# Kernel optimization log

Hardware: AMD Instinct MI355X
Metric: run time of the kernel (lower is better)

## Reference

```python
import jax, jax.numpy as jnp
import numpy as np

TEMPERATURE = 10000.0
LN_EPS = 1e-5

def build_freqs(H, W, head_dim):
    # (H*W, head_dim) rotary angles: [theta_h, theta_h, theta_w, theta_w]
    gh, gw = jnp.meshgrid(jnp.arange(H, dtype=jnp.float32), jnp.arange(W, dtype=jnp.float32), indexing='ij')
    dq = head_dim // 4
    freq = 1.0 / (TEMPERATURE ** (jnp.arange(dq, dtype=jnp.float32) / dq))
    th = gh.reshape(-1, 1) * freq[None, :]
    tw = gw.reshape(-1, 1) * freq[None, :]
    return jnp.concatenate([th, th, tw, tw], axis=-1)

def apply_rope(x, freqs):
    # x: (B, nh, N, hd), freqs: (N, hd)
    cos = jnp.cos(freqs)[None, None]
    sin = jnp.sin(freqs)[None, None]
    hd = x.shape[-1]
    x1, x2 = x[..., :hd // 2], x[..., hd // 2:]
    x_rot = jnp.concatenate([-x2, x1], axis=-1)
    return x * cos + x_rot * sin

def setup_inputs() -> dict:
    key = jax.random.key(0)
    ks = jax.random.split(key, 8)
    dim, hidden, B, H, W = 192, 384, 4, 128, 128
    N = H * W
    s = 0.02
    return {
        'x': jax.random.normal(ks[0], (B, N, dim), jnp.float32),
        'in_w': jax.random.normal(ks[1], (hidden, dim), jnp.float32) * s,
        'in_b': jnp.zeros((hidden,), jnp.float32),
        'qkv_w': jax.random.normal(ks[2], (3 * hidden, hidden), jnp.float32) * s,
        'qkv_b': jnp.zeros((3 * hidden,), jnp.float32),
        'lepe_w': jax.random.normal(ks[3], (hidden, 1, 3, 3), jnp.float32) * s,
        'lepe_b': jnp.zeros((hidden,), jnp.float32),
        'ln_g': jnp.ones((hidden,), jnp.float32),
        'ln_b': jnp.zeros((hidden,), jnp.float32),
        'out_w': jax.random.normal(ks[4], (dim, hidden), jnp.float32) * s,
        'out_b': jnp.zeros((dim,), jnp.float32),
        'H': H,
        'W': W,
    }

def reference(x, in_w, in_b, qkv_w, qkv_b, lepe_w, lepe_b, ln_g, ln_b, out_w, out_b, H, W):
    B, N, C = x.shape
    hidden = in_w.shape[0]
    nh = 8
    hd = hidden // nh
    # in_proj: 1x1 conv == per-token linear
    x_seq = jnp.einsum('bnc,hc->bnh', x, in_w) + in_b
    # fused qkv
    qkv = jnp.einsum('bnh,oh->bno', x_seq, qkv_w) + qkv_b
    q, k, v = jnp.split(qkv, 3, axis=-1)
    # LEPE: 3x3 depthwise conv on V in NCHW layout
    v2d = v.transpose(0, 2, 1).reshape(B, hidden, H, W)
    lepe = jax.lax.conv_general_dilated(
        v2d, lepe_w, window_strides=(1, 1), padding=((1, 1), (1, 1)),
        feature_group_count=hidden, dimension_numbers=('NCHW', 'OIHW', 'NCHW'))
    lepe = lepe + lepe_b[None, :, None, None]
    v = v + lepe.reshape(B, hidden, N).transpose(0, 2, 1)
    # split heads -> (B, nh, N, hd)
    q = q.reshape(B, N, nh, hd).transpose(0, 2, 1, 3)
    k = k.reshape(B, N, nh, hd).transpose(0, 2, 1, 3)
    v = v.reshape(B, N, nh, hd).transpose(0, 2, 1, 3)
    freqs = build_freqs(H, W, hd)
    q = apply_rope(q, freqs)
    k = apply_rope(k, freqs)
    # phi = ELU + 1 feature map
    q = jax.nn.elu(q) + 1.0
    k = jax.nn.elu(k) + 1.0
    # linear attention associativity trick
    kv = jnp.einsum('bhnd,bhne->bhde', k, v)
    out = jnp.einsum('bhnd,bhde->bhne', q, kv)
    k_sum = k.sum(axis=2)  # (B, nh, hd)
    denom = jnp.maximum(jnp.einsum('bhnd,bhd->bhn', q, k_sum)[..., None], 1e-6)
    out = out / denom
    out = out.transpose(0, 2, 1, 3).reshape(B, N, hidden)
    # LayerNorm + out_proj
    mu = out.mean(axis=-1, keepdims=True)
    var = out.var(axis=-1, keepdims=True)
    out = (out - mu) * jax.lax.rsqrt(var + LN_EPS) * ln_g + ln_b
    return jnp.einsum('bnh,ch->bnc', out, out_w) + out_b
```

## Files before the change

kernel.cpp:

```cpp
#include <hip/hip_runtime.h>
#include <cstdint>
#include <cstddef>

#define NN_TOK 16384
#define ROWS   65536
#define CDIM   192
#define HID    384
#define NHEAD  8
#define HD     48
#define QKVO   1152

typedef unsigned short ushort_t;
typedef __bf16 bf16x8 __attribute__((ext_vector_type(8)));
typedef float  f32x4  __attribute__((ext_vector_type(4)));

__device__ __forceinline__ ushort_t f2bf(float f) {
  unsigned int u = __float_as_uint(f);
  u += 0x7fffu + ((u >> 16) & 1u);
  return (ushort_t)(u >> 16);
}
__device__ __forceinline__ float bf2f(ushort_t u) {
  return __uint_as_float(((unsigned int)u) << 16);
}

__global__ void cast_x(const float* __restrict__ x, ushort_t* __restrict__ xb, int n8) {
  int i = blockIdx.x * blockDim.x + threadIdx.x;
  if (i >= n8) return;
  const float4* src = (const float4*)(x + (size_t)i * 8);
  float4 f0 = src[0], f1 = src[1];
  uint4 pk;
  pk.x = (unsigned)f2bf(f0.x) | ((unsigned)f2bf(f0.y) << 16);
  pk.y = (unsigned)f2bf(f0.z) | ((unsigned)f2bf(f0.w) << 16);
  pk.z = (unsigned)f2bf(f1.x) | ((unsigned)f2bf(f1.y) << 16);
  pk.w = (unsigned)f2bf(f1.z) | ((unsigned)f2bf(f1.w) << 16);
  *(uint4*)(xb + (size_t)i * 8) = pk;
}

__global__ void combine_w(const float* __restrict__ in_w, const float* __restrict__ in_b,
                          const float* __restrict__ qkv_w, const float* __restrict__ qkv_b,
                          ushort_t* __restrict__ Wcb, float* __restrict__ bc) {
  int o = blockIdx.x;
  int c = threadIdx.x;
  const float* qw = qkv_w + o * HID;
  float s = 0.f;
  for (int m = 0; m < HID; ++m) s += qw[m] * in_w[m * CDIM + c];
  Wcb[o * CDIM + c] = f2bf(s);
  if (c == 0) {
    float sb = qkv_b[o];
    for (int m = 0; m < HID; ++m) sb += qw[m] * in_b[m];
    bc[o] = sb;
  }
}

__global__ void cast_ow(const float* __restrict__ w, ushort_t* __restrict__ wb, int n) {
  int i = blockIdx.x * blockDim.x + threadIdx.x;
  if (i < n) wb[i] = f2bf(w[i]);
}

__global__ void build_tab(float4* __restrict__ tab4) {
  int i = blockIdx.x * blockDim.x + threadIdx.x;
  if (i >= NN_TOK * 24) return;
  int n = i / 24, dp = i - n * 24;
  int j = dp % 12;
  const float c0 = 1.1073093649624542f;
  float freq = exp2f(-(float)j * c0);
  float fy = (float)(n >> 7), fx = (float)(n & 127);
  float s1, c1, s2, c2;
  sincosf(fy * freq, &s1, &c1);
  sincosf(fx * freq, &s2, &c2);
  tab4[i] = make_float4(c1, s1, c2, s2);
}

template<int BM, int BN, int WM, int WN, bool OUTBF16>
__global__ __launch_bounds__(256) void gemm_mfma(const ushort_t* __restrict__ A, int lda,
                                                 const ushort_t* __restrict__ Wb,
                                                 const float* __restrict__ bias,
                                                 void* __restrict__ Cptr,
                                                 int K, int O) {
  constexpr int TM = BM / WM / 16;
  constexpr int TN = BN / WN / 16;
  __shared__ __align__(16) ushort_t As[BM][40];
  __shared__ __align__(16) ushort_t Bs[BN][40];
  const int t    = threadIdx.x;
  const int lane = t & 63;
  const int wave = t >> 6;
  const int quad = lane >> 4;
  const int l15  = lane & 15;
  const int wm   = wave / WN, wn = wave % WN;
  const int m_base = wm * (BM / WM);
  const int n_base = wn * (BN / WN);
  const int n0 = blockIdx.y * BM;
  const int o0 = blockIdx.x * BN;
  f32x4 acc[TM][TN] = {};

  for (int kt = 0; kt < K; kt += 32) {
    for (int c = t; c < BM * 4; c += 256) {
      int row = c >> 2, col8 = (c & 3) * 8;
      *(uint4*)&As[row][col8] = *(const uint4*)(A + (size_t)(n0 + row) * lda + kt + col8);
    }
    for (int c = t; c < BN * 4; c += 256) {
      int row = c >> 2, col8 = (c & 3) * 8;
      *(uint4*)&Bs[row][col8] = *(const uint4*)(Wb + (size_t)(o0 + row) * K + kt + col8);
    }
    __syncthreads();
    bf16x8 af[TM], bfr[TN];
#pragma unroll
    for (int mi = 0; mi < TM; ++mi)
      af[mi] = *(const bf16x8*)&As[m_base + mi * 16 + l15][quad * 8];
#pragma unroll
    for (int ni = 0; ni < TN; ++ni)
      bfr[ni] = *(const bf16x8*)&Bs[n_base + ni * 16 + l15][quad * 8];
#pragma unroll
    for (int mi = 0; mi < TM; ++mi)
#pragma unroll
      for (int ni = 0; ni < TN; ++ni)
        acc[mi][ni] = __builtin_amdgcn_mfma_f32_16x16x32_bf16(af[mi], bfr[ni], acc[mi][ni], 0, 0, 0);
    __syncthreads();
  }
#pragma unroll
  for (int mi = 0; mi < TM; ++mi) {
#pragma unroll
    for (int ni = 0; ni < TN; ++ni) {
      int col = o0 + n_base + ni * 16 + l15;
      float bv = bias[col];
      int rbase = n0 + m_base + mi * 16 + quad * 4;
#pragma unroll
      for (int r = 0; r < 4; ++r) {
        float val = acc[mi][ni][r] + bv;
        if (OUTBF16) ((ushort_t*)Cptr)[(size_t)(rbase + r) * O + col] = f2bf(val);
        else         ((float*)Cptr)[(size_t)(rbase + r) * O + col] = val;
      }
    }
  }
}

__global__ __launch_bounds__(256) void kv_partial_k(const ushort_t* __restrict__ kq,
                                                    const ushort_t* __restrict__ vq,
                                                    const float4* __restrict__ tab4,
                                                    const float* __restrict__ lw,
                                                    const float* __restrict__ lb,
                                                    float* __restrict__ part) {
  const int bid   = blockIdx.x;
  const int chunk = bid & 63;
  const int bh    = bid >> 6;
  const int b     = bh >> 3;
  const int h     = bh & 7;
  const int t     = threadIdx.x;
  const int lane  = t & 63;
  const int wave  = t >> 6;
  __shared__ __align__(16) ushort_t ksF[3][16][16][8];
  __shared__ __align__(16) ushort_t vsF[3][16][16][8];
  __shared__ float wlds[9][48];
  __shared__ float blds[48];
  float* red   = (float*)&ksF[0][0][0][0];
  float* ksred = (float*)&vsF[0][0][0][0];
  for (int c = t; c < 432; c += 256) {
    int ch = c / 9, tap = c - ch * 9;
    wlds[tap][ch] = lw[(h * HD + ch) * 9 + tap];
  }
  if (t < 48) blds[t] = lb[h * HD + t];
  __syncthreads();

  const int g  = lane >> 4;
  const int d0 = lane & 15;
  f32x4 acc[3][3] = {};
  float ksacc = 0.f;
  const int n0 = b * NN_TOK + chunk * 256;

  for (int it = 0; it < 2; ++it) {
    const int nbase = it * 128;
    for (int c = t; c < 384; c += 256) {
      int rr = c / 3, s8 = (c - (c / 3) * 3) * 8;
      int n  = n0 + nbase + rr;
      int nn = n & (NN_TOK - 1);
      const ushort_t* kr = kq + (size_t)n * QKVO + h * HD;
      uint4 ka = *(const uint4*)(kr + s8);
      uint4 kb = *(const uint4*)(kr + s8 + 24);
      ushort_t ua[8], ub[8];
      *(uint4*)ua = ka; *(uint4*)ub = kb;
      const float4* t4 = tab4 + nn * 24 + s8;
      const int nb = rr >> 3, nm = rr & 7;
#pragma unroll
      for (int jj = 0; jj < 8; ++jj) {
        float4 cs = t4[jj];
        float in1 = bf2f(ua[jj]), in2 = bf2f(ub[jj]);
        float o1 = in1 * cs.x - in2 * cs.y;
        float o2 = in2 * cs.z + in1 * cs.w;
        o1 = (o1 > 0.f) ? o1 + 1.f : expf(o1);
        o2 = (o2 > 0.f) ? o2 + 1.f : expf(o2);
        const int d1 = s8 + jj, d2 = s8 + 24 + jj;
        ksF[d1 >> 4][nb][d1 & 15][nm] = f2bf(o1);
        ksF[d2 >> 4][nb][d2 & 15][nm] = f2bf(o2);
      }
    }
    {
      const int nst = chunk * 256 + nbase;
      const int y   = nst >> 7;
      for (int c = t; c < 768; c += 256) {
        int rr = c / 6, gg = c - (c / 6) * 6;
        int x = rr;
        float a8[8], ctr[8];
#pragma unroll
        for (int ci = 0; ci < 8; ++ci) a8[ci] = blds[gg * 8 + ci];
#pragma unroll
        for (int dy = -1; dy <= 1; ++dy) {
#pragma unroll
          for (int dx = -1; dx <= 1; ++dx) {
            int yy = y + dy, xx = x + dx;
            float m = ((unsigned)yy < 128u && (unsigned)xx < 128u) ? 1.f : 0.f;
            int yc = min(max(yy, 0), 127), xc = min(max(xx, 0), 127);
            const ushort_t* src = vq + ((size_t)(b * NN_TOK + (yc << 7) + xc)) * QKVO + h * HD + gg * 8;
            uint4 pk = *(const uint4*)src;
            ushort_t uu[8];
            *(uint4*)uu = pk;
            const int tap = (dy + 1) * 3 + (dx + 1);
#pragma unroll
            for (int ci = 0; ci < 8; ++ci) {
              float val = bf2f(uu[ci]);
              if (dy == 0 && dx == 0) ctr[ci] = val;
              a8[ci] += (wlds[tap][gg * 8 + ci] * m) * val;
            }
          }
        }
        const int nb = rr >> 3, nm = rr & 7;
#pragma unroll
        for (int ci = 0; ci < 8; ++ci) {
          const int e = gg * 8 + ci;
          vsF[e >> 4][nb][e & 15][nm] = f2bf(ctr[ci] + a8[ci]);
        }
      }
    }
    __syncthreads();
    {
      const int w4 = wave * 4 + g;
      bf16x8 af[3], bfr[3];
#pragma unroll
      for (int dg = 0; dg < 3; ++dg) af[dg]  = *(const bf16x8*)&ksF[dg][w4][d0][0];
#pragma unroll
      for (int eg = 0; eg < 3; ++eg) bfr[eg] = *(const bf16x8*)&vsF[eg][w4][d0][0];
#pragma unroll
      for (int dg = 0; dg < 3; ++dg)
#pragma unroll
        for (int eg = 0; eg < 3; ++eg)
          acc[dg][eg] = __builtin_amdgcn_mfma_f32_16x16x32_bf16(af[dg], bfr[eg], acc[dg][eg], 0, 0, 0);
    }
    if (lane < 48) {
      const int dg = lane >> 4, dd = lane & 15;
#pragma unroll 8
      for (int rr = 0; rr < 32; ++rr) {
        int nl = wave * 32 + rr;
        ksacc += bf2f(ksF[dg][nl >> 3][dd][nl & 7]);
      }
    }
    __syncthreads();
  }
  if (wave == 0) {
#pragma unroll
    for (int dg = 0; dg < 3; ++dg)
#pragma unroll
      for (int eg = 0; eg < 3; ++eg)
#pragma unroll
        for (int r = 0; r < 4; ++r)
          red[(dg * 16 + g * 4 + r) * 48 + eg * 16 + d0] = acc[dg][eg][r];
  }
  if (lane < 48) ksred[wave * 48 + lane] = ksacc;
  __syncthreads();
  for (int w = 1; w < 4; ++w) {
    if (wave == w) {
#pragma unroll
      for (int dg = 0; dg < 3; ++dg)
#pragma unroll
        for (int eg = 0; eg < 3; ++eg)
#pragma unroll
          for (int r = 0; r < 4; ++r)
            red[(dg * 16 + g * 4 + r) * 48 + eg * 16 + d0] += acc[dg][eg][r];
    }
    __syncthreads();
  }
  float* p = part + (size_t)bid * 2352;
  for (int c = t; c < 2304; c += 256) p[c] = red[c];
  if (t < 48) p[2304 + t] = ksred[t] + ksred[48 + t] + ksred[96 + t] + ksred[144 + t];
}

__global__ void kv_phase2(const float* __restrict__ part, ushort_t* __restrict__ kvT) {
  int bh  = blockIdx.x >> 3;
  int seg = blockIdx.x & 7;
  int t   = threadIdx.x;
  ushort_t* dst = kvT + (size_t)bh * 8192;
  for (int i = seg * 1024 + t; i < (seg + 1) * 1024; i += 256) {
    int rem = i & 4095, e = rem >> 6, d = rem & 63;
    if (d >= 48 || e >= 49) dst[i] = 0;
  }
  int cend = (seg + 1) * 294;
  for (int c = seg * 294 + t; c < cend; c += 256) {
    const float* p = part + (size_t)(bh * 64) * 2352 + c;
    float s = 0.f;
    for (int ch = 0; ch < 64; ++ch) s += p[(size_t)ch * 2352];
    int d, e;
    if (c < 2304) { d = c / 48; e = c - d * 48; }
    else          { e = 48; d = c - 2304; }
    ushort_t hi = f2bf(s);
    float lo = s - bf2f(hi);
    dst[(size_t)e * 64 + d]        = hi;
    dst[4096 + (size_t)e * 64 + d] = f2bf(lo);
  }
}

__global__ __launch_bounds__(256) void attn_ln_fused(const ushort_t* __restrict__ q,
                                                     const float4* __restrict__ tab4,
                                                     const ushort_t* __restrict__ kvT,
                                                     const float* __restrict__ ln_g,
                                                     const float* __restrict__ ln_b,
                                                     ushort_t* __restrict__ oln) {
  __shared__ __align__(16) ushort_t qsL[32][392];
  __shared__ float lnp[4][32][2];
  const int t    = threadIdx.x;
  const int lane = t & 63;
  const int wave = t >> 6;
  const int quad = lane >> 4;
  const int l15  = lane & 15;
  const int row0 = blockIdx.x * 32;
  const int b    = row0 >> 14;
  const int h0   = wave * 2;
  const float2* tab2 = (const float2*)tab4;

  for (int c = t; c < 1536; c += 256) {
    int r = c / 48, seg = c - (c / 48) * 48;
    *(uint4*)&qsL[r][seg * 8] = *(const uint4*)(q + (size_t)(row0 + r) * QKVO + seg * 8);
  }
  __syncthreads();

  f32x4 acc[2][2][4] = {};

  float gg[2][3], bb[2][3];
#pragma unroll
  for (int hi = 0; hi < 2; ++hi)
#pragma unroll
    for (int nt = 0; nt < 3; ++nt) {
      int col = (h0 + hi) * 48 + nt * 16 + l15;
      gg[hi][nt] = ln_g[col];
      bb[hi][nt] = ln_b[col];
    }

#pragma unroll
  for (int s = 0; s < 2; ++s) {
    const int d0 = s * 32 + quad * 8;
    const bool valid = d0 < 48;
    const bool caseA = d0 < 24;
    const int dp0 = caseA ? d0 : d0 - 24;
    bf16x8 af[2][2] = {};
    if (valid) {
      const int dpart = caseA ? d0 + 24 : d0 - 24;
      const int csel  = caseA ? 0 : 1;
      const float sgn = caseA ? -1.f : 1.f;
#pragma unroll
      for (int m = 0; m < 2; ++m) {
        const int r  = row0 + m * 16 + l15;
        const int nn = r & (NN_TOK - 1);
        float2 cs[8];
#pragma unroll
        for (int j = 0; j < 8; ++j) cs[j] = tab2[(size_t)(nn * 24 + dp0 + j) * 2 + csel];
#pragma unroll
        for (int hi = 0; hi < 2; ++hi) {
          const ushort_t* qr = &qsL[m * 16 + l15][(h0 + hi) * 48];
          uint4 pr = *(const uint4*)(qr + d0);
          uint4 pa = *(const uint4*)(qr + dpart);
          ushort_t up[8], ua[8];
          *(uint4*)up = pr; *(uint4*)ua = pa;
          unsigned w[4];
#pragma unroll
          for (int j2 = 0; j2 < 4; ++j2) {
            float o2[2];
#pragma unroll
            for (int k = 0; k < 2; ++k) {
              int j = j2 * 2 + k;
              float vp = bf2f(up[j]), va = bf2f(ua[j]);
              float o = vp * cs[j].x + va * (sgn * cs[j].y);
              o2[k] = (o > 0.f) ? o + 1.f : expf(o);
            }
            w[j2] = (unsigned)f2bf(o2[0]) | ((unsigned)f2bf(o2[1]) << 16);
          }
          uint4 pk = make_uint4(w[0], w[1], w[2], w[3]);
          af[hi][m] = *(bf16x8*)&pk;
        }
      }
    }
#pragma unroll
    for (int hi = 0; hi < 2; ++hi) {
      const ushort_t* kb = kvT + (size_t)(b * 8 + h0 + hi) * 8192;
#pragma unroll
      for (int nt = 0; nt < 4; ++nt) {
        bf16x8 bH = *(const bf16x8*)(kb + (nt * 16 + l15) * 64 + d0);
        bf16x8 bL = *(const bf16x8*)(kb + 4096 + (nt * 16 + l15) * 64 + d0);
#pragma unroll
        for (int m = 0; m < 2; ++m) {
          acc[hi][m][nt] = __builtin_amdgcn_mfma_f32_16x16x32_bf16(af[hi][m], bH, acc[hi][m][nt], 0, 0, 0);
          acc[hi][m][nt] = __builtin_amdgcn_mfma_f32_16x16x32_bf16(af[hi][m], bL, acc[hi][m][nt], 0, 0, 0);
        }
      }
    }
  }

  float rdn[2][2][4];
#pragma unroll
  for (int hi = 0; hi < 2; ++hi)
#pragma unroll
    for (int m = 0; m < 2; ++m)
#pragma unroll
      for (int r = 0; r < 4; ++r) {
        float dn = __shfl(acc[hi][m][3][r], lane & 48);
        rdn[hi][m][r] = 1.f / fmaxf(dn, 1e-6f);
      }
  float s1[2][4] = {}, s2[2][4] = {};
#pragma unroll
  for (int hi = 0; hi < 2; ++hi)
#pragma unroll
    for (int m = 0; m < 2; ++m)
#pragma unroll
      for (int nt = 0; nt < 3; ++nt)
#pragma unroll
        for (int r = 0; r < 4; ++r) {
          float o = acc[hi][m][nt][r] * rdn[hi][m][r];
          acc[hi][m][nt][r] = o;
          s1[m][r] += o;
          s2[m][r] += o * o;
        }
#pragma unroll
  for (int m = 0; m < 2; ++m)
#pragma unroll
    for (int r = 0; r < 4; ++r) {
#pragma unroll
      for (int msk = 1; msk < 16; msk <<= 1) {
        s1[m][r] += __shfl_xor(s1[m][r], msk, 64);
        s2[m][r] += __shfl_xor(s2[m][r], msk, 64);
      }
    }
  if (l15 == 0) {
#pragma unroll
    for (int m = 0; m < 2; ++m)
#pragma unroll
      for (int r = 0; r < 4; ++r) {
        int rr = m * 16 + quad * 4 + r;
        lnp[wave][rr][0] = s1[m][r];
        lnp[wave][rr][1] = s2[m][r];
      }
  }
  __syncthreads();
  float muv[2][4], rsv[2][4];
#pragma unroll
  for (int m = 0; m < 2; ++m)
#pragma unroll
    for (int r = 0; r < 4; ++r) {
      int rr = m * 16 + quad * 4 + r;
      float a  = lnp[0][rr][0] + lnp[1][rr][0] + lnp[2][rr][0] + lnp[3][rr][0];
      float bq = lnp[0][rr][1] + lnp[1][rr][1] + lnp[2][rr][1] + lnp[3][rr][1];
      float mu  = a * (1.f / 384.f);
      float var = bq * (1.f / 384.f) - mu * mu;
      muv[m][r] = mu;
      rsv[m][r] = rsqrtf(var + 1e-5f);
    }
#pragma unroll
  for (int hi = 0; hi < 2; ++hi)
#pragma unroll
    for (int m = 0; m < 2; ++m)
#pragma unroll
      for (int nt = 0; nt < 3; ++nt) {
        int col = (h0 + hi) * 48 + nt * 16 + l15;
#pragma unroll
        for (int r = 0; r < 4; ++r) {
          int rr = m * 16 + quad * 4 + r;
          float v = (acc[hi][m][nt][r] - muv[m][r]) * rsv[m][r] * gg[hi][nt] + bb[hi][nt];
          qsL[rr][col] = f2bf(v);
        }
      }
  __syncthreads();
  for (int c = t; c < 1536; c += 256) {
    int r = c / 48, seg = c - (c / 48) * 48;
    *(uint4*)(oln + (size_t)(row0 + r) * QKVO + seg * 8) = *(const uint4*)&qsL[r][seg * 8];
  }
}

extern "C" void kernel_launch(void* const* d_in, const int* in_sizes, int n_in,
                              void* d_out, int out_size, void* d_ws, size_t ws_size,
                              hipStream_t stream) {
  const float* x      = (const float*)d_in[0];
  const float* in_w   = (const float*)d_in[1];
  const float* in_b   = (const float*)d_in[2];
  const float* qkv_w  = (const float*)d_in[3];
  const float* qkv_b  = (const float*)d_in[4];
  const float* lepe_w = (const float*)d_in[5];
  const float* lepe_b = (const float*)d_in[6];
  const float* ln_g   = (const float*)d_in[7];
  const float* ln_b   = (const float*)d_in[8];
  const float* out_w  = (const float*)d_in[9];
  const float* out_b  = (const float*)d_in[10];
  float* out = (float*)d_out;

  float*    ws     = (float*)d_ws;
  float*    qkvbF  = ws;
  float*    xbF    = qkvbF + (size_t)ROWS * QKVO / 2;
  float*    WcbF   = xbF   + (size_t)ROWS * CDIM / 2;
  float*    bc     = WcbF  + (size_t)QKVO * CDIM / 2;
  float*    owbF   = bc    + QKVO;
  float*    tab4F  = owbF  + (size_t)CDIM * HID / 2;
  ushort_t* qkvb   = (ushort_t*)qkvbF;
  ushort_t* xb     = (ushort_t*)xbF;
  float*    part   = xbF;
  ushort_t* kvT    = (ushort_t*)(xbF + (size_t)2048 * 2352);
  ushort_t* Wcb    = (ushort_t*)WcbF;
  ushort_t* owb    = (ushort_t*)owbF;
  float4*   tab4   = (float4*)tab4F;

  cast_x<<<(ROWS * CDIM / 8 + 255) / 256, 256, 0, stream>>>(x, xb, ROWS * CDIM / 8);
  combine_w<<<QKVO, CDIM, 0, stream>>>(in_w, in_b, qkv_w, qkv_b, Wcb, bc);
  cast_ow<<<(CDIM * HID + 255) / 256, 256, 0, stream>>>(out_w, owb, CDIM * HID);
  build_tab<<<(NN_TOK * 24 + 255) / 256, 256, 0, stream>>>(tab4);

  dim3 gqkv(QKVO / 128, ROWS / 128);
  gemm_mfma<128, 128, 2, 2, true><<<gqkv, 256, 0, stream>>>(xb, CDIM, Wcb, bc, qkvb, CDIM, QKVO);

  kv_partial_k<<<2048, 256, 0, stream>>>(qkvb + HID, qkvb + 2 * HID, tab4, lepe_w, lepe_b, part);
  kv_phase2<<<256, 256, 0, stream>>>(part, kvT);

  attn_ln_fused<<<ROWS / 32, 256, 0, stream>>>(qkvb, tab4, kvT, ln_g, ln_b, qkvb + HID);

  dim3 g6(CDIM / 64, ROWS / 128);
  gemm_mfma<128, 64, 4, 1, false><<<g6, 256, 0, stream>>>(qkvb + HID, QKVO, owb, out_b, out, HID, CDIM);
}
```

Before: 437.5 us.

## Fuse fp32-to-bf16 input cast into QKV GEMM and swizzle block order for XCDs

Removes the separate cast_x kernel by having the QKV GEMM load fp32 x directly and convert it to bf16 while staging the A tile into shared memory. This saves the bf16 copy of x being written and then read back, at the cost of reading twice the bytes per A tile inside the GEMM. The grid is also flattened to 1D and its block IDs remapped so that consecutive tiles land on the same XCD, which should improve L2 reuse of shared operand tiles on the chiplet layout. The fp32 A tile is re-read and re-converted by every column block (9 of them), so more global traffic goes to the GEMM in exchange for dropping one launch.

```diff
diff --git a/kernel.cpp b/kernel.cpp
--- a/kernel.cpp
+++ b/kernel.cpp
@@ -21,19 +21,6 @@
 }
 __device__ __forceinline__ float bf2f(ushort_t u) {
   return __uint_as_float(((unsigned int)u) << 16);
-}
-
-__global__ void cast_x(const float* __restrict__ x, ushort_t* __restrict__ xb, int n8) {
-  int i = blockIdx.x * blockDim.x + threadIdx.x;
-  if (i >= n8) return;
-  const float4* src = (const float4*)(x + (size_t)i * 8);
-  float4 f0 = src[0], f1 = src[1];
-  uint4 pk;
-  pk.x = (unsigned)f2bf(f0.x) | ((unsigned)f2bf(f0.y) << 16);
-  pk.y = (unsigned)f2bf(f0.z) | ((unsigned)f2bf(f0.w) << 16);
-  pk.z = (unsigned)f2bf(f1.x) | ((unsigned)f2bf(f1.y) << 16);
-  pk.w = (unsigned)f2bf(f1.z) | ((unsigned)f2bf(f1.w) << 16);
-  *(uint4*)(xb + (size_t)i * 8) = pk;
 }
 
 __global__ void combine_w(const float* __restrict__ in_w, const float* __restrict__ in_b,
@@ -71,12 +58,12 @@
   tab4[i] = make_float4(c1, s1, c2, s2);
 }
 
-template<int BM, int BN, int WM, int WN, bool OUTBF16>
-__global__ __launch_bounds__(256) void gemm_mfma(const ushort_t* __restrict__ A, int lda,
+template<int BM, int BN, int WM, int WN, bool OUTBF16, bool AF32>
+__global__ __launch_bounds__(256) void gemm_mfma(const void* __restrict__ A, int lda,
                                                  const ushort_t* __restrict__ Wb,
                                                  const float* __restrict__ bias,
                                                  void* __restrict__ Cptr,
-                                                 int K, int O) {
+                                                 int K, int O, int nbx) {
   constexpr int TM = BM / WM / 16;
   constexpr int TN = BN / WN / 16;
   __shared__ __align__(16) ushort_t As[BM][40];
@@ -89,14 +76,29 @@
   const int wm   = wave / WN, wn = wave % WN;
   const int m_base = wm * (BM / WM);
   const int n_base = wn * (BN / WN);
-  const int n0 = blockIdx.y * BM;
-  const int o0 = blockIdx.x * BN;
+  const int cpx = gridDim.x >> 3;
+  const int id  = blockIdx.x;
+  const int swz = (id & 7) * cpx + (id >> 3);
+  const int o0  = (swz % nbx) * BN;
+  const int n0  = (swz / nbx) * BM;
   f32x4 acc[TM][TN] = {};
 
   for (int kt = 0; kt < K; kt += 32) {
     for (int c = t; c < BM * 4; c += 256) {
       int row = c >> 2, col8 = (c & 3) * 8;
-      *(uint4*)&As[row][col8] = *(const uint4*)(A + (size_t)(n0 + row) * lda + kt + col8);
+      if constexpr (AF32) {
+        const float* Af = (const float*)A + (size_t)(n0 + row) * lda + kt + col8;
+        float4 f0 = ((const float4*)Af)[0], f1 = ((const float4*)Af)[1];
+        uint4 pk;
+        pk.x = (unsigned)f2bf(f0.x) | ((unsigned)f2bf(f0.y) << 16);
+        pk.y = (unsigned)f2bf(f0.z) | ((unsigned)f2bf(f0.w) << 16);
+        pk.z = (unsigned)f2bf(f1.x) | ((unsigned)f2bf(f1.y) << 16);
+        pk.w = (unsigned)f2bf(f1.z) | ((unsigned)f2bf(f1.w) << 16);
+        *(uint4*)&As[row][col8] = pk;
+      } else {
+        *(uint4*)&As[row][col8] =
+            *(const uint4*)((const ushort_t*)A + (size_t)(n0 + row) * lda + kt + col8);
+      }
     }
     for (int c = t; c < BN * 4; c += 256) {
       int row = c >> 2, col8 = (c & 3) * 8;
@@ -498,32 +500,30 @@
 
   float*    ws     = (float*)d_ws;
   float*    qkvbF  = ws;
-  float*    xbF    = qkvbF + (size_t)ROWS * QKVO / 2;
-  float*    WcbF   = xbF   + (size_t)ROWS * CDIM / 2;
+  float*    scratch= qkvbF + (size_t)ROWS * QKVO / 2;
+  float*    WcbF   = scratch + (size_t)ROWS * CDIM / 2;
   float*    bc     = WcbF  + (size_t)QKVO * CDIM / 2;
   float*    owbF   = bc    + QKVO;
   float*    tab4F  = owbF  + (size_t)CDIM * HID / 2;
   ushort_t* qkvb   = (ushort_t*)qkvbF;
-  ushort_t* xb     = (ushort_t*)xbF;
-  float*    part   = xbF;
-  ushort_t* kvT    = (ushort_t*)(xbF + (size_t)2048 * 2352);
+  float*    part   = scratch;
+  ushort_t* kvT    = (ushort_t*)(scratch + (size_t)2048 * 2352);
   ushort_t* Wcb    = (ushort_t*)WcbF;
   ushort_t* owb    = (ushort_t*)owbF;
   float4*   tab4   = (float4*)tab4F;
 
-  cast_x<<<(ROWS * CDIM / 8 + 255) / 256, 256, 0, stream>>>(x, xb, ROWS * CDIM / 8);
   combine_w<<<QKVO, CDIM, 0, stream>>>(in_w, in_b, qkv_w, qkv_b, Wcb, bc);
   cast_ow<<<(CDIM * HID + 255) / 256, 256, 0, stream>>>(out_w, owb, CDIM * HID);
   build_tab<<<(NN_TOK * 24 + 255) / 256, 256, 0, stream>>>(tab4);
 
-  dim3 gqkv(QKVO / 128, ROWS / 128);
-  gemm_mfma<128, 128, 2, 2, true><<<gqkv, 256, 0, stream>>>(xb, CDIM, Wcb, bc, qkvb, CDIM, QKVO);
+  gemm_mfma<128, 128, 2, 2, true, true><<<4608, 256, 0, stream>>>(
+      x, CDIM, Wcb, bc, qkvb, CDIM, QKVO, 9);
 
   kv_partial_k<<<2048, 256, 0, stream>>>(qkvb + HID, qkvb + 2 * HID, tab4, lepe_w, lepe_b, part);
   kv_phase2<<<256, 256, 0, stream>>>(part, kvT);
 
   attn_ln_fused<<<ROWS / 32, 256, 0, stream>>>(qkvb, tab4, kvT, ln_g, ln_b, qkvb + HID);
 
-  dim3 g6(CDIM / 64, ROWS / 128);
-  gemm_mfma<128, 64, 4, 1, false><<<g6, 256, 0, stream>>>(qkvb + HID, QKVO, owb, out_b, out, HID, CDIM);
-}
+  gemm_mfma<128, 64, 4, 1, false, false><<<1536, 256, 0, stream>>>(
+      qkvb + HID, QKVO, owb, out_b, out, HID, CDIM, 3);
+}
```

Result: no change. 445.6 us (+1.8%).
